# Performance work log

Hardware: AMD Instinct MI355X
Metric: run time of the kernel (lower is better)

## Reference

```python
import jax, jax.numpy as jnp
import numpy as np

N_NODES = 40000
N_EDGES = 640000
IN, HID, OUT = 128, 128, 47


def setup_inputs() -> dict:
    key = jax.random.key(0)
    ks = jax.random.split(key, 12)
    def glorot(k, shape):
        fan = sum(shape)
        return jax.random.normal(k, shape, dtype=jnp.float32) * jnp.sqrt(2.0 / fan)
    return {
        "x": jax.random.normal(ks[0], (N_NODES, IN), dtype=jnp.float32),
        "src": jax.random.randint(ks[1], (N_EDGES,), 0, N_NODES),
        "dst": jax.random.randint(ks[2], (N_EDGES,), 0, N_NODES),
        "W_self0": glorot(ks[3], (IN, HID)),
        "W_neigh0": glorot(ks[4], (IN, HID)),
        "b0": jnp.zeros((HID,), dtype=jnp.float32),
        "W_self1": glorot(ks[5], (HID, HID)),
        "W_neigh1": glorot(ks[6], (HID, HID)),
        "b1": jnp.zeros((HID,), dtype=jnp.float32),
        "W_self2": glorot(ks[7], (HID, OUT)),
        "W_neigh2": glorot(ks[8], (HID, OUT)),
        "b2": jnp.zeros((OUT,), dtype=jnp.float32),
    }


def _sage_conv(h, src, dst, W_self, W_neigh, b):
    # DGL SAGEConv('mean'): mean of neighbor (src) feats scattered to dst,
    # then fc_neigh(h_neigh) + fc_self(h_self) + bias.
    n = h.shape[0]
    deg = jax.ops.segment_sum(jnp.ones_like(dst, dtype=h.dtype), dst, num_segments=n)
    agg = jax.ops.segment_sum(h[src], dst, num_segments=n)          # [N, d] gather + scatter-add
    h_neigh = agg / jnp.maximum(deg, 1.0)[:, None]                   # isolated nodes -> 0 (DGL behavior)
    return h @ W_self + h_neigh @ W_neigh + b


def reference(x, src, dst, W_self0, W_neigh0, b0, W_self1, W_neigh1, b1,
              W_self2, W_neigh2, b2):
    # Dropout is identity in eval mode; omitted here.
    h = _sage_conv(x, src, dst, W_self0, W_neigh0, b0)
    h = jax.nn.relu(h)
    h = _sage_conv(h, src, dst, W_self1, W_neigh1, b1)
    h = jax.nn.relu(h)
    h = _sage_conv(h, src, dst, W_self2, W_neigh2, b2)
    return h
```

## Files before the change

### kernel.cpp

```cpp
#include <hip/hip_runtime.h>
#include <hip/hip_bf16.h>
#include <stdint.h>

#define NN 40000
#define NE 640000
#define NB 157

typedef __attribute__((ext_vector_type(8))) short bf16x8;
typedef __attribute__((ext_vector_type(4))) float f32x4;
typedef __attribute__((ext_vector_type(2))) float f32x2v;

static __device__ __forceinline__ unsigned short f2b(float f) {
    unsigned b = __float_as_uint(f);
    return (unsigned short)((b + 0x7FFFu + ((b >> 16) & 1u)) >> 16);
}
static __device__ __forceinline__ float blo(unsigned v) { return __uint_as_float(v << 16); }
static __device__ __forceinline__ float bhi(unsigned v) { return __uint_as_float(v & 0xffff0000u); }

static __device__ __forceinline__ void acc4(float* a, uint2 v) {
    a[0] += blo(v.x); a[1] += bhi(v.x);
    a[2] += blo(v.y); a[3] += bhi(v.y);
}


#if __has_builtin(__builtin_amdgcn_cvt_pk_fp8_f32) && __has_builtin(__builtin_amdgcn_cvt_pk_f32_fp8)
#define FP8_HW 1
#else
#define FP8_HW 0
#endif

static __device__ __forceinline__ unsigned char f2fp8_sw(float f) {
    f = fminf(fmaxf(f, -448.f), 448.f);
    unsigned b = __float_as_uint(f);
    unsigned s = (b >> 24) & 0x80u;
    unsigned ab = b & 0x7fffffffu;
    if (ab < 0x3c000000u) return (unsigned char)s;
    unsigned r = ab + 0x7ffffu + ((ab >> 20) & 1u);
    unsigned e = ((r >> 23) - 120u) & 0xfu;
    unsigned m = (r >> 20) & 7u;
    return (unsigned char)(s | (e << 3) | m);
}
static __device__ __forceinline__ float fp82f_sw(unsigned char u) {
    unsigned s = ((unsigned)u & 0x80u) << 24;
    unsigned e = (u >> 3) & 15u, m = u & 7u;
    float nrm = __uint_as_float(s | ((e + 120u) << 23) | (m << 20));
    float dnm = __uint_as_float(s | 0x3f800000u) * (float)m * 0.001953125f;
    return e ? nrm : dnm;
}

static __device__ __forceinline__ unsigned pack_fp8x4(float a, float b, float c, float d) {
#if FP8_HW
    int v = __builtin_amdgcn_cvt_pk_fp8_f32(a, b, 0, false);
    v = __builtin_amdgcn_cvt_pk_fp8_f32(c, d, v, true);
    return (unsigned)v;
#else
    return (unsigned)f2fp8_sw(a) | ((unsigned)f2fp8_sw(b) << 8) |
           ((unsigned)f2fp8_sw(c) << 16) | ((unsigned)f2fp8_sw(d) << 24);
#endif
}

static __device__ __forceinline__ void acc4f8(float* a, unsigned v) {
#if FP8_HW
    f32x2v p0 = __builtin_amdgcn_cvt_pk_f32_fp8((int)v, false);
    f32x2v p1 = __builtin_amdgcn_cvt_pk_f32_fp8((int)v, true);
    a[0] += p0.x; a[1] += p0.y; a[2] += p1.x; a[3] += p1.y;
#else
    a[0] += fp82f_sw(v & 0xff);         a[1] += fp82f_sw((v >> 8) & 0xff);
    a[2] += fp82f_sw((v >> 16) & 0xff); a[3] += fp82f_sw(v >> 24);
#endif
}
static __device__ __forceinline__ void acc16f8(float* a, uint4 v) {
    acc4f8(a, v.x); acc4f8(a + 4, v.y); acc4f8(a + 8, v.z); acc4f8(a + 12, v.w);
}


__global__ void count_deg_kernel(const int* __restrict__ dst, int* __restrict__ deg, int n) {
    int i = blockIdx.x * blockDim.x + threadIdx.x;
    if (i < n) atomicAdd(&deg[dst[i]], 1);
}

__global__ __launch_bounds__(256) void scan1_kernel(const int* __restrict__ deg,
                                                    int* __restrict__ bsum) {
    int i = blockIdx.x * 256 + threadIdx.x;
    int v = (i < NN) ? deg[i] : 0;
#pragma unroll
    for (int off = 1; off < 64; off <<= 1) v += __shfl_xor(v, off);
    __shared__ int ws4[4];
    if ((threadIdx.x & 63) == 0) ws4[threadIdx.x >> 6] = v;
    __syncthreads();
    if (threadIdx.x == 0) bsum[blockIdx.x] = ws4[0] + ws4[1] + ws4[2] + ws4[3];
}

__global__ void scan_top_kernel(const int* __restrict__ bsum, int* __restrict__ btop) {
    int lane = threadIdx.x;
    int run = 0;
    for (int base = 0; base < NB; base += 64) {
        int idx = base + lane;
        int v = (idx < NB) ? bsum[idx] : 0;
        int s = v;
#pragma unroll
        for (int off = 1; off < 64; off <<= 1) { int t = __shfl_up(s, off); if (lane >= off) s += t; }
        if (idx < NB) btop[idx] = run + s - v;
        run += __shfl(s, 63);
    }
}

__global__ __launch_bounds__(256) void scan2_kernel(const int* __restrict__ deg,
                                                    const int* __restrict__ btop,
                                                    int* __restrict__ row_ptr) {
    int b = blockIdx.x;
    int i = b * 256 + threadIdx.x;
    int lane = threadIdx.x & 63, wv = threadIdx.x >> 6;
    int v = (i < NN) ? deg[i] : 0;
    int s = v;
#pragma unroll
    for (int off = 1; off < 64; off <<= 1) { int t = __shfl_up(s, off); if (lane >= off) s += t; }
    __shared__ int wsum[4];
    if (lane == 63) wsum[wv] = s;
    __syncthreads();
    int add = btop[b];
    for (int w = 0; w < wv; ++w) add += wsum[w];
    if (i < NN) row_ptr[i] = add + s - v;
    if (i == NN - 1) row_ptr[NN] = add + s;
}

__global__ void fill_csr_kernel(const int* __restrict__ src, const int* __restrict__ dst,
                                const int* __restrict__ row_ptr, int* __restrict__ cursor,
                                int* __restrict__ csr, int n) {
    int i = blockIdx.x * blockDim.x + threadIdx.x;
    if (i < n) {
        int d = dst[i];
        int pos = row_ptr[d] + atomicAdd(&cursor[d], 1);
        csr[pos] = src[i];
    }
}


__global__ __launch_bounds__(256) void prep_kernel(
    const float* __restrict__ x,
    const float* __restrict__ Ws0, const float* __restrict__ Wn0,
    const float* __restrict__ Ws1, const float* __restrict__ Wn1,
    const float* __restrict__ Ws2, const float* __restrict__ Wn2,
    int* __restrict__ zero_base, unsigned short* __restrict__ X,
    unsigned char* __restrict__ X8,
    unsigned short* __restrict__ Wt0, unsigned short* __restrict__ Wt1,
    unsigned short* __restrict__ Wt2s, unsigned short* __restrict__ Wt2n) {
    int b = blockIdx.x, tid = threadIdx.x;
    if (b < 79) {
        int i = (b * 256 + tid) * 4;
        if (i < 80000) *(int4*)(zero_base + i) = (int4){0, 0, 0, 0};
    } else if (b < 5079) {
        int i = (b - 79) * 256 + tid;
        int e = i << 2;
        float4 v = *(const float4*)(x + e);
        uint2 o;
        o.x = f2b(v.x) | ((unsigned)f2b(v.y) << 16);
        o.y = f2b(v.z) | ((unsigned)f2b(v.w) << 16);
        *(uint2*)(X + e) = o;
        *(unsigned*)(X8 + e) = pack_fp8x4(v.x, v.y, v.z, v.w);
    } else {
        int i = (b - 5079) * 256 + tid;
        if (i < 65536) {
            int l = i >> 15, j = i & 32767;
            int n = j >> 8, k = j & 255;
            const float* Ws = l ? Ws1 : Ws0;
            const float* Wn = l ? Wn1 : Wn0;
            float v = (k < 128) ? Ws[k * 128 + n] : Wn[(k - 128) * 128 + n];
            (l ? Wt1 : Wt0)[n * 256 + k] = f2b(v);
        } else if (i < 65536 + 6144) {
            int j = i - 65536;
            int n = j >> 7, k = j & 127;
            float v = (n < 47) ? Ws2[k * 47 + n] : 0.f;
            Wt2s[n * 128 + k] = f2b(v);
        } else if (i < 65536 + 12288) {
            int j = i - 65536 - 6144;
            int n = j >> 7, k = j & 127;
            float v = (n < 47) ? Wn2[k * 47 + n] : 0.f;
            Wt2n[n * 128 + k] = f2b(v);
        }
    }
}


template <bool RELU, bool WFP8>
__global__ __launch_bounds__(256) void sage_layer_kernel(
    const unsigned short* __restrict__ Hin, const unsigned char* __restrict__ H8in,
    const int* __restrict__ csr, const int* __restrict__ row_ptr,
    const unsigned short* __restrict__ Wt, const float* __restrict__ bias,
    unsigned short* __restrict__ Hout, unsigned char* __restrict__ H8out) {
    __shared__ unsigned short agg_lds[16 * 128];

    int tid = threadIdx.x;
    int wv = tid >> 6, lane = tid & 63;
    int lr = lane & 15, lg = lane >> 4;
    int lr8 = lane & 7, eg8 = lane >> 3;
    int m0 = blockIdx.x * 16;

    int nb = m0 + wv * 4;
    int rp5 = (lane < 5) ? row_ptr[nb + lane] : 0;
    for (int t = 0; t < 4; ++t) {
        int beg = __shfl(rp5, t), end = __shfl(rp5, t + 1);
        float a[16] = {};
        int j = beg + eg8;
        for (; j + 8 < end; j += 16) {
            int s0 = csr[j], s1 = csr[j + 8];
            uint4 v0 = *(const uint4*)(H8in + (size_t)s0 * 128 + lr8 * 16);
            uint4 v1 = *(const uint4*)(H8in + (size_t)s1 * 128 + lr8 * 16);
            acc16f8(a, v0); acc16f8(a, v1);
        }
        if (j < end) {
            uint4 v = *(const uint4*)(H8in + (size_t)csr[j] * 128 + lr8 * 16);
            acc16f8(a, v);
        }
#pragma unroll
        for (int k = 0; k < 16; ++k) {
            a[k] += __shfl_xor(a[k], 8);
            a[k] += __shfl_xor(a[k], 16);
            a[k] += __shfl_xor(a[k], 32);
        }
        if (eg8 == 0) {
            float inv = 1.0f / fmaxf((float)(end - beg), 1.0f);
            uint4 o0, o1;
            o0.x = f2b(a[0] * inv)  | ((unsigned)f2b(a[1] * inv) << 16);
            o0.y = f2b(a[2] * inv)  | ((unsigned)f2b(a[3] * inv) << 16);
            o0.z = f2b(a[4] * inv)  | ((unsigned)f2b(a[5] * inv) << 16);
            o0.w = f2b(a[6] * inv)  | ((unsigned)f2b(a[7] * inv) << 16);
            o1.x = f2b(a[8] * inv)  | ((unsigned)f2b(a[9] * inv) << 16);
            o1.y = f2b(a[10] * inv) | ((unsigned)f2b(a[11] * inv) << 16);
            o1.z = f2b(a[12] * inv) | ((unsigned)f2b(a[13] * inv) << 16);
            o1.w = f2b(a[14] * inv) | ((unsigned)f2b(a[15] * inv) << 16);
            int row = wv * 4 + t;
            *(uint4*)&agg_lds[row * 128 + ((2 * lr8) ^ row) * 8] = o0;
            *(uint4*)&agg_lds[row * 128 + ((2 * lr8 + 1) ^ row) * 8] = o1;
        }
    }
    __syncthreads();

    bf16x8 afr[8];
#pragma unroll
    for (int kt = 0; kt < 4; ++kt)
        afr[kt] = *(const bf16x8*)(Hin + (size_t)(m0 + lr) * 128 + kt * 32 + lg * 8);
#pragma unroll
    for (int kt = 0; kt < 4; ++kt) {
        int chunk = (kt * 4 + lg) ^ lr;
        afr[4 + kt] = *(const bf16x8*)&agg_lds[lr * 128 + chunk * 8];
    }

    int n0 = (wv * 2) * 16 + lr;
    int n1 = n0 + 16;
    f32x4 acc0 = (f32x4){0.f, 0.f, 0.f, 0.f};
    f32x4 acc1 = (f32x4){0.f, 0.f, 0.f, 0.f};
#pragma unroll
    for (int kt = 0; kt < 8; ++kt) {
        bf16x8 b0 = *(const bf16x8*)(Wt + (size_t)n0 * 256 + kt * 32 + lg * 8);
        bf16x8 b1 = *(const bf16x8*)(Wt + (size_t)n1 * 256 + kt * 32 + lg * 8);
        acc0 = __builtin_amdgcn_mfma_f32_16x16x32_bf16(afr[kt], b0, acc0, 0, 0, 0);
        acc1 = __builtin_amdgcn_mfma_f32_16x16x32_bf16(afr[kt], b1, acc1, 0, 0, 0);
    }

    float bs0 = bias[n0], bs1 = bias[n1];
#pragma unroll
    for (int r = 0; r < 4; ++r) {
        int m = m0 + lg * 4 + r;
        float v0 = acc0[r] + bs0;
        float v1 = acc1[r] + bs1;
        if (RELU) { v0 = fmaxf(v0, 0.f); v1 = fmaxf(v1, 0.f); }
        Hout[(size_t)m * 128 + n0] = f2b(v0);
        Hout[(size_t)m * 128 + n1] = f2b(v1);
        if (WFP8) {
#if FP8_HW
            H8out[(size_t)m * 128 + n0] =
                (unsigned char)(__builtin_amdgcn_cvt_pk_fp8_f32(v0, v0, 0, false) & 0xff);
            H8out[(size_t)m * 128 + n1] =
                (unsigned char)(__builtin_amdgcn_cvt_pk_fp8_f32(v1, v1, 0, false) & 0xff);
#else
            H8out[(size_t)m * 128 + n0] = f2fp8_sw(v0);
            H8out[(size_t)m * 128 + n1] = f2fp8_sw(v1);
#endif
        }
    }
}


__global__ __launch_bounds__(192) void dual_gemm_kernel(
    const unsigned short* __restrict__ H2,
    const unsigned short* __restrict__ Wt2s, const unsigned short* __restrict__ Wt2n,
    const float* __restrict__ b2,
    float* __restrict__ out, unsigned short* __restrict__ Hn) {
    int wv = threadIdx.x >> 6, lane = threadIdx.x & 63;
    int lr = lane & 15, lg = lane >> 4;

    bf16x8 bfr[2][4];
    float bs[2];
#pragma unroll
    for (int c = 0; c < 2; ++c) {
        int t = wv * 2 + c;
        bool is_s = t < 3;
        int n = (is_s ? t : t - 3) * 16 + lr;
        const unsigned short* W = is_s ? Wt2s : Wt2n;
#pragma unroll
        for (int kt = 0; kt < 4; ++kt)
            bfr[c][kt] = *(const bf16x8*)(W + (size_t)n * 128 + kt * 32 + lg * 8);
        bs[c] = (is_s && n < 47) ? b2[n] : 0.f;
    }

    for (int tt = 0; tt < 2; ++tt) {
        int m0 = blockIdx.x * 32 + tt * 16;
        bf16x8 afr[4];
#pragma unroll
        for (int kt = 0; kt < 4; ++kt)
            afr[kt] = *(const bf16x8*)(H2 + (size_t)(m0 + lr) * 128 + kt * 32 + lg * 8);
        f32x4 acc[2];
#pragma unroll
        for (int c = 0; c < 2; ++c) acc[c] = (f32x4){0.f, 0.f, 0.f, 0.f};
#pragma unroll
        for (int kt = 0; kt < 4; ++kt)
#pragma unroll
            for (int c = 0; c < 2; ++c)
                acc[c] = __builtin_amdgcn_mfma_f32_16x16x32_bf16(afr[kt], bfr[c][kt], acc[c], 0, 0, 0);
#pragma unroll
        for (int c = 0; c < 2; ++c) {
            int t = wv * 2 + c;
            bool is_s = t < 3;
            int n = (is_s ? t : t - 3) * 16 + lr;
#pragma unroll
            for (int r = 0; r < 4; ++r) {
                int m = m0 + lg * 4 + r;
                float v = acc[c][r] + bs[c];
                if (is_s) {
                    if (n < 47) out[(size_t)m * 47 + n] = v;
                } else {
                    Hn[(size_t)m * 48 + n] = f2b(v);
                }
            }
        }
    }
}


__global__ void aggregate_out_kernel(const unsigned short* __restrict__ Hn,
                                     const int* __restrict__ csr,
                                     const int* __restrict__ row_ptr,
                                     float* __restrict__ out) {
    int node = (blockIdx.x * blockDim.x + threadIdx.x) >> 6;
    int lane = threadIdx.x & 63;
    if (node >= NN) return;
    int eg = lane >> 4, lc = lane & 15;
    int beg = row_ptr[node], end = row_ptr[node + 1];
    float a[4] = {};
    int j = beg + eg;
    for (; j + 12 < end; j += 16) {
        int s0 = csr[j], s1 = csr[j + 4], s2 = csr[j + 8], s3 = csr[j + 12];
        uint2 v0 = *(const uint2*)(Hn + (size_t)s0 * 48 + lc * 4);
        uint2 v1 = *(const uint2*)(Hn + (size_t)s1 * 48 + lc * 4);
        uint2 v2 = *(const uint2*)(Hn + (size_t)s2 * 48 + lc * 4);
        uint2 v3 = *(const uint2*)(Hn + (size_t)s3 * 48 + lc * 4);
        acc4(a, v0); acc4(a, v1); acc4(a, v2); acc4(a, v3);
    }
    for (; j < end; j += 4) {
        uint2 v = *(const uint2*)(Hn + (size_t)csr[j] * 48 + lc * 4);
        acc4(a, v);
    }
#pragma unroll
    for (int k = 0; k < 4; ++k) {
        a[k] += __shfl_xor(a[k], 16);
        a[k] += __shfl_xor(a[k], 32);
    }
    if (eg == 0 && lc < 12) {
        float inv = 1.0f / fmaxf((float)(end - beg), 1.0f);
        int c0 = lc * 4;
#pragma unroll
        for (int r = 0; r < 4; ++r)
            if (c0 + r < 47) out[(size_t)node * 47 + c0 + r] += a[r] * inv;
    }
}


extern "C" void kernel_launch(void* const* d_in, const int* in_sizes, int n_in,
                              void* d_out, int out_size, void* d_ws, size_t ws_size,
                              hipStream_t stream) {
    const float* x   = (const float*)d_in[0];
    const int*   src = (const int*)d_in[1];
    const int*   dst = (const int*)d_in[2];
    const float* Ws0 = (const float*)d_in[3];
    const float* Wn0 = (const float*)d_in[4];
    const float* b0  = (const float*)d_in[5];
    const float* Ws1 = (const float*)d_in[6];
    const float* Wn1 = (const float*)d_in[7];
    const float* b1  = (const float*)d_in[8];
    const float* Ws2 = (const float*)d_in[9];
    const float* Wn2 = (const float*)d_in[10];
    const float* b2  = (const float*)d_in[11];
    float* out = (float*)d_out;

    uintptr_t p = ((uintptr_t)d_ws + 255) & ~(uintptr_t)255;
    auto take = [&](size_t bytes) {
        void* r = (void*)p;
        p = (p + bytes + 255) & ~(uintptr_t)255;
        return r;
    };
    int* deg     = (int*)take(40000 * 4);
    int* cursor  = (int*)take(40000 * 4);
    int* row_ptr = (int*)take(40004 * 4);
    int* csr     = (int*)take(640000 * 4);
    unsigned short* X   = (unsigned short*)take((size_t)NN * 128 * 2);
    unsigned short* H1  = (unsigned short*)take((size_t)NN * 128 * 2);
    unsigned short* H2  = X;
    unsigned short* Wt0 = (unsigned short*)take(128 * 256 * 2);
    unsigned short* Wt1 = (unsigned short*)take(128 * 256 * 2);
    unsigned short* Wt2s = (unsigned short*)take(48 * 128 * 2);
    unsigned short* Wt2n = (unsigned short*)take(48 * 128 * 2);
    unsigned short* Hn  = (unsigned short*)take(((size_t)NN * 48 + 64) * 2);
    int* bsum = (int*)take(NB * 4);
    int* btop = (int*)take(NB * 4);
    unsigned char* X8  = (unsigned char*)take((size_t)NN * 128);
    unsigned char* H18 = (unsigned char*)take((size_t)NN * 128);

    prep_kernel<<<5383, 256, 0, stream>>>(x, Ws0, Wn0, Ws1, Wn1, Ws2, Wn2,
                                          deg, X, X8, Wt0, Wt1, Wt2s, Wt2n);
    count_deg_kernel<<<2500, 256, 0, stream>>>(dst, deg, NE);
    scan1_kernel<<<NB, 256, 0, stream>>>(deg, bsum);
    scan_top_kernel<<<1, 64, 0, stream>>>(bsum, btop);
    scan2_kernel<<<NB, 256, 0, stream>>>(deg, btop, row_ptr);
    fill_csr_kernel<<<2500, 256, 0, stream>>>(src, dst, row_ptr, cursor, csr, NE);

    sage_layer_kernel<true, true><<<2500, 256, 0, stream>>>(X, X8, csr, row_ptr, Wt0, b0, H1, H18);
    sage_layer_kernel<true, false><<<2500, 256, 0, stream>>>(H1, H18, csr, row_ptr, Wt1, b1, H2, nullptr);
    dual_gemm_kernel<<<1250, 192, 0, stream>>>(H2, Wt2s, Wt2n, b2, out, Hn);
    aggregate_out_kernel<<<10000, 256, 0, stream>>>(Hn, csr, row_ptr, out);
}
```

Before: 210.6 us.

## Process four nodes per wave concurrently in aggregation with padded zero row

The neighbor aggregation in the layer kernel now assigns each wave's four destination nodes to separate 16-lane groups that run at the same time, with each node's edge range split across two 8-lane halves. The old version looped over the nodes one after another. The inner loop issues four gathers per iteration, and out-of-range slots are redirected to an extra zeroed row at index NN, which removes tail branches and cuts the shuffle reduction to one step. The Hn stride is also padded from 48 to 64 elements for aligned rows. In exchange there is more load imbalance between lanes when node degrees differ, and some gathers read the dummy row.

```diff
diff --git a/kernel.cpp b/kernel.cpp
--- a/kernel.cpp
+++ b/kernel.cpp
@@ -142,7 +142,7 @@
     const float* __restrict__ Ws1, const float* __restrict__ Wn1,
     const float* __restrict__ Ws2, const float* __restrict__ Wn2,
     int* __restrict__ zero_base, unsigned short* __restrict__ X,
-    unsigned char* __restrict__ X8,
+    unsigned char* __restrict__ X8, unsigned char* __restrict__ H18,
     unsigned short* __restrict__ Wt0, unsigned short* __restrict__ Wt1,
     unsigned short* __restrict__ Wt2s, unsigned short* __restrict__ Wt2n) {
     int b = blockIdx.x, tid = threadIdx.x;
@@ -158,7 +158,7 @@
         o.y = f2b(v.z) | ((unsigned)f2b(v.w) << 16);
         *(uint2*)(X + e) = o;
         *(unsigned*)(X8 + e) = pack_fp8x4(v.x, v.y, v.z, v.w);
-    } else {
+    } else if (b < 5383) {
         int i = (b - 5079) * 256 + tid;
         if (i < 65536) {
             int l = i >> 15, j = i & 32767;
@@ -178,6 +178,9 @@
             float v = (n < 47) ? Wn2[k * 47 + n] : 0.f;
             Wt2n[n * 128 + k] = f2b(v);
         }
+    } else {
+        if (tid < 16) *(uint2*)(X8 + (size_t)NN * 128 + tid * 8) = (uint2){0, 0};
+        else if (tid < 32) *(uint2*)(H18 + (size_t)NN * 128 + (tid - 16) * 8) = (uint2){0, 0};
     }
 }
 
@@ -193,46 +196,52 @@
     int tid = threadIdx.x;
     int wv = tid >> 6, lane = tid & 63;
     int lr = lane & 15, lg = lane >> 4;
-    int lr8 = lane & 7, eg8 = lane >> 3;
+    int lr8 = lane & 7, g = lane >> 3;
+    int t = g >> 1, sub = g & 1;
     int m0 = blockIdx.x * 16;
 
     int nb = m0 + wv * 4;
     int rp5 = (lane < 5) ? row_ptr[nb + lane] : 0;
-    for (int t = 0; t < 4; ++t) {
-        int beg = __shfl(rp5, t), end = __shfl(rp5, t + 1);
-        float a[16] = {};
-        int j = beg + eg8;
-        for (; j + 8 < end; j += 16) {
-            int s0 = csr[j], s1 = csr[j + 8];
-            uint4 v0 = *(const uint4*)(H8in + (size_t)s0 * 128 + lr8 * 16);
-            uint4 v1 = *(const uint4*)(H8in + (size_t)s1 * 128 + lr8 * 16);
-            acc16f8(a, v0); acc16f8(a, v1);
-        }
-        if (j < end) {
-            uint4 v = *(const uint4*)(H8in + (size_t)csr[j] * 128 + lr8 * 16);
-            acc16f8(a, v);
-        }
-#pragma unroll
-        for (int k = 0; k < 16; ++k) {
-            a[k] += __shfl_xor(a[k], 8);
-            a[k] += __shfl_xor(a[k], 16);
-            a[k] += __shfl_xor(a[k], 32);
-        }
-        if (eg8 == 0) {
-            float inv = 1.0f / fmaxf((float)(end - beg), 1.0f);
-            uint4 o0, o1;
-            o0.x = f2b(a[0] * inv)  | ((unsigned)f2b(a[1] * inv) << 16);
-            o0.y = f2b(a[2] * inv)  | ((unsigned)f2b(a[3] * inv) << 16);
-            o0.z = f2b(a[4] * inv)  | ((unsigned)f2b(a[5] * inv) << 16);
-            o0.w = f2b(a[6] * inv)  | ((unsigned)f2b(a[7] * inv) << 16);
-            o1.x = f2b(a[8] * inv)  | ((unsigned)f2b(a[9] * inv) << 16);
-            o1.y = f2b(a[10] * inv) | ((unsigned)f2b(a[11] * inv) << 16);
-            o1.z = f2b(a[12] * inv) | ((unsigned)f2b(a[13] * inv) << 16);
-            o1.w = f2b(a[14] * inv) | ((unsigned)f2b(a[15] * inv) << 16);
-            int row = wv * 4 + t;
-            *(uint4*)&agg_lds[row * 128 + ((2 * lr8) ^ row) * 8] = o0;
-            *(uint4*)&agg_lds[row * 128 + ((2 * lr8 + 1) ^ row) * 8] = o1;
-        }
+    int beg = __shfl(rp5, t), end = __shfl(rp5, t + 1);
+    int deg = end - beg;
+    int half = (deg + 1) >> 1;
+    int js = beg + sub * half;
+    int je = sub ? end : beg + half;
+    int last = (je > js) ? je - 1 : js;
+
+    float a[16] = {};
+    for (int j = js; j < je; j += 4) {
+        int j1 = j + 1, j2 = j + 2, j3 = j + 3;
+        int iA = csr[j];
+        int iBr = csr[min(j1, last)];
+        int iCr = csr[min(j2, last)];
+        int iDr = csr[min(j3, last)];
+        int iB = (j1 < je) ? iBr : NN;
+        int iC = (j2 < je) ? iCr : NN;
+        int iD = (j3 < je) ? iDr : NN;
+        uint4 vA = *(const uint4*)(H8in + (size_t)iA * 128 + lr8 * 16);
+        uint4 vB = *(const uint4*)(H8in + (size_t)iB * 128 + lr8 * 16);
+        uint4 vC = *(const uint4*)(H8in + (size_t)iC * 128 + lr8 * 16);
+        uint4 vD = *(const uint4*)(H8in + (size_t)iD * 128 + lr8 * 16);
+        acc16f8(a, vA); acc16f8(a, vB); acc16f8(a, vC); acc16f8(a, vD);
+    }
+#pragma unroll
+    for (int k = 0; k < 16; ++k) a[k] += __shfl_xor(a[k], 8);
+
+    if (sub == 0) {
+        float inv = 1.0f / fmaxf((float)deg, 1.0f);
+        uint4 o0, o1;
+        o0.x = f2b(a[0] * inv)  | ((unsigned)f2b(a[1] * inv) << 16);
+        o0.y = f2b(a[2] * inv)  | ((unsigned)f2b(a[3] * inv) << 16);
+        o0.z = f2b(a[4] * inv)  | ((unsigned)f2b(a[5] * inv) << 16);
+        o0.w = f2b(a[6] * inv)  | ((unsigned)f2b(a[7] * inv) << 16);
+        o1.x = f2b(a[8] * inv)  | ((unsigned)f2b(a[9] * inv) << 16);
+        o1.y = f2b(a[10] * inv) | ((unsigned)f2b(a[11] * inv) << 16);
+        o1.z = f2b(a[12] * inv) | ((unsigned)f2b(a[13] * inv) << 16);
+        o1.w = f2b(a[14] * inv) | ((unsigned)f2b(a[15] * inv) << 16);
+        int row = wv * 4 + t;
+        *(uint4*)&agg_lds[row * 128 + ((2 * lr8) ^ row) * 8] = o0;
+        *(uint4*)&agg_lds[row * 128 + ((2 * lr8 + 1) ^ row) * 8] = o1;
     }
     __syncthreads();
 
@@ -330,7 +339,7 @@
                 if (is_s) {
                     if (n < 47) out[(size_t)m * 47 + n] = v;
                 } else {
-                    Hn[(size_t)m * 48 + n] = f2b(v);
+                    Hn[(size_t)m * 64 + n] = f2b(v);
                 }
             }
         }
@@ -351,14 +360,14 @@
     int j = beg + eg;
     for (; j + 12 < end; j += 16) {
         int s0 = csr[j], s1 = csr[j + 4], s2 = csr[j + 8], s3 = csr[j + 12];
-        uint2 v0 = *(const uint2*)(Hn + (size_t)s0 * 48 + lc * 4);
-        uint2 v1 = *(const uint2*)(Hn + (size_t)s1 * 48 + lc * 4);
-        uint2 v2 = *(const uint2*)(Hn + (size_t)s2 * 48 + lc * 4);
-        uint2 v3 = *(const uint2*)(Hn + (size_t)s3 * 48 + lc * 4);
+        uint2 v0 = *(const uint2*)(Hn + (size_t)s0 * 64 + lc * 4);
+        uint2 v1 = *(const uint2*)(Hn + (size_t)s1 * 64 + lc * 4);
+        uint2 v2 = *(const uint2*)(Hn + (size_t)s2 * 64 + lc * 4);
+        uint2 v3 = *(const uint2*)(Hn + (size_t)s3 * 64 + lc * 4);
         acc4(a, v0); acc4(a, v1); acc4(a, v2); acc4(a, v3);
     }
     for (; j < end; j += 4) {
-        uint2 v = *(const uint2*)(Hn + (size_t)csr[j] * 48 + lc * 4);
+        uint2 v = *(const uint2*)(Hn + (size_t)csr[j] * 64 + lc * 4);
         acc4(a, v);
     }
 #pragma unroll
@@ -410,14 +419,14 @@
     unsigned short* Wt1 = (unsigned short*)take(128 * 256 * 2);
     unsigned short* Wt2s = (unsigned short*)take(48 * 128 * 2);
     unsigned short* Wt2n = (unsigned short*)take(48 * 128 * 2);
-    unsigned short* Hn  = (unsigned short*)take(((size_t)NN * 48 + 64) * 2);
+    unsigned short* Hn  = (unsigned short*)take((size_t)NN * 64 * 2);
     int* bsum = (int*)take(NB * 4);
     int* btop = (int*)take(NB * 4);
-    unsigned char* X8  = (unsigned char*)take((size_t)NN * 128);
-    unsigned char* H18 = (unsigned char*)take((size_t)NN * 128);
-
-    prep_kernel<<<5383, 256, 0, stream>>>(x, Ws0, Wn0, Ws1, Wn1, Ws2, Wn2,
-                                          deg, X, X8, Wt0, Wt1, Wt2s, Wt2n);
+    unsigned char* X8  = (unsigned char*)take((size_t)(NN + 1) * 128);
+    unsigned char* H18 = (unsigned char*)take((size_t)(NN + 1) * 128);
+
+    prep_kernel<<<5384, 256, 0, stream>>>(x, Ws0, Wn0, Ws1, Wn1, Ws2, Wn2,
+                                          deg, X, X8, H18, Wt0, Wt1, Wt2s, Wt2n);
     count_deg_kernel<<<2500, 256, 0, stream>>>(dst, deg, NE);
     scan1_kernel<<<NB, 256, 0, stream>>>(deg, bsum);
     scan_top_kernel<<<1, 64, 0, stream>>>(bsum, btop);
```

Result: faster. 181.2 us (-14.0%).
